# Optimization experiments

Measured on AMD Instinct MI355X. Metric: run time of the kernel, lower is better.

## Reference

```python
import jax, jax.numpy as jnp
import numpy as np

ROPE_THETA = 10000.0

def apply_rope(x, pos):
    # x: [..., h, s, d], pos: [s] int positions
    d = x.shape[-1]
    inv_freq = ROPE_THETA ** (-jnp.arange(0, d, 2, dtype=jnp.float32) / d)  # [d/2]
    ang = pos.astype(jnp.float32)[:, None] * inv_freq[None, :]              # [s, d/2]
    cos, sin = jnp.cos(ang), jnp.sin(ang)
    x1, x2 = x[..., 0::2], x[..., 1::2]
    r1 = x1 * cos - x2 * sin
    r2 = x1 * sin + x2 * cos
    return jnp.stack([r1, r2], axis=-1).reshape(x.shape)

def setup_inputs() -> dict:
    key = jax.random.key(0)
    ks = jax.random.split(key, 5)
    B, S, D = 2, 2048, 1024
    scale = 1.0 / np.sqrt(D)
    return {
        "x": jax.random.normal(ks[0], (B, S, D), dtype=jnp.float32),
        "token_position": jnp.arange(S, dtype=jnp.int32),
        "Wq": jax.random.normal(ks[1], (D, D), dtype=jnp.float32) * scale,
        "Wk": jax.random.normal(ks[2], (D, D), dtype=jnp.float32) * scale,
        "Wv": jax.random.normal(ks[3], (D, D), dtype=jnp.float32) * scale,
        "Wo": jax.random.normal(ks[4], (D, D), dtype=jnp.float32) * scale,
    }

def reference(x, token_position, Wq, Wk, Wv, Wo):
    H = 16
    B, S, D = x.shape
    ds = D // H
    def split_heads(t):  # [b,s,(h d)] -> [b,h,s,d]
        return t.reshape(B, S, H, ds).transpose(0, 2, 1, 3)
    Q = split_heads(x @ Wq.T)
    K = split_heads(x @ Wk.T)
    V = split_heads(x @ Wv.T)
    Q = apply_rope(Q, token_position)
    K = apply_rope(K, token_position)
    scores = jnp.einsum('bhqd,bhkd->bhqk', Q, K) / jnp.sqrt(jnp.float32(ds))
    causal = jnp.tril(jnp.ones((S, S), dtype=bool))
    scores = jnp.where(causal, scores, jnp.finfo(scores.dtype).min)
    attn = jax.nn.softmax(scores, axis=-1)
    out = jnp.einsum('bhqk,bhkd->bhqd', attn, V)
    out = out.transpose(0, 2, 1, 3).reshape(B, S, D)
    return out @ Wo.T
```

## Files before the change

### kernel.cpp

```cpp
#include <hip/hip_runtime.h>
#include <math.h>

#define BB 2
#define SS 2048
#define DD 1024
#define HH 16
#define M_TOTAL (BB*SS)

typedef __attribute__((ext_vector_type(8))) short bf16x8;
typedef __attribute__((ext_vector_type(4))) float f32x4;

__device__ __forceinline__ short f2bf(float f) {
    union { float f; unsigned u; } v; v.f = f;
    unsigned r = v.u + 0x7fffu + ((v.u >> 16) & 1u);
    return (short)(r >> 16);
}
__device__ __forceinline__ float bf2f(short h) {
    union { unsigned u; float f; } v; v.u = ((unsigned)(unsigned short)h) << 16;
    return v.f;
}
__device__ __forceinline__ unsigned cvt_pk_bf16(float lo, float hi) {
    unsigned r;
    asm volatile("v_cvt_pk_bf16_f32 %0, %1, %2" : "=v"(r) : "v"(lo), "v"(hi));
    return r;
}
__device__ __forceinline__ void gload16(const void* g, void* l) {
    __builtin_amdgcn_global_load_lds(
        (const __attribute__((address_space(1))) unsigned int*)g,
        (__attribute__((address_space(3))) unsigned int*)l, 16, 0, 0);
}

__global__ __launch_bounds__(256) void cvt_bf16(const float* __restrict__ in,
                                                short* __restrict__ out, int n,
                                                float scale)
{
    int i = (blockIdx.x * 256 + threadIdx.x) * 4;
    if (i >= n) return;
    float4 v = *(const float4*)(in + i);
    short4 o;
    o.x = f2bf(v.x * scale); o.y = f2bf(v.y * scale);
    o.z = f2bf(v.z * scale); o.w = f2bf(v.w * scale);
    *(short4*)(out + i) = o;
}

template<int BN, int OUT_BF16>
__global__ __launch_bounds__(256) void gemm_nt_mfma(const short* __restrict__ A,
                                                    const short* __restrict__ W0,
                                                    const short* __restrict__ W1,
                                                    const short* __restrict__ W2,
                                                    void* __restrict__ C0,
                                                    void* __restrict__ C1,
                                                    void* __restrict__ C2,
                                                    int M, int N, int K)
{
    constexpr int WC = BN / 64;
    constexpr int WR = 4 / WC;
    constexpr int MW = 128 / WR;
    constexpr int MT = MW / 16;

    __shared__ __align__(16) short As[128 * 64];
    __shared__ __align__(16) short Bs[BN * 64];

    const short* W = (blockIdx.z == 0) ? W0 : (blockIdx.z == 1) ? W1 : W2;
    void* Cout     = (blockIdx.z == 0) ? C0 : (blockIdx.z == 1) ? C1 : C2;

    const int tid = threadIdx.x;
    const int lane = tid & 63;
    const int w = tid >> 6;
    const int lg = lane >> 4, lc = lane & 15;
    const int wr = w / WC, wc = w % WC;
    const int m0 = blockIdx.x * 128, n0 = blockIdx.y * BN;
    const int wbase = (tid & 0xC0) * 8;

    f32x4 acc[MT][4] = {};

    for (int k0 = 0; k0 < K; k0 += 64) {
        __syncthreads();
#pragma unroll
        for (int it = 0; it < 4; ++it) {
            int cl = it * 256 + tid;
            int r = cl >> 3;
            int c = (cl & 7) ^ (r & 7);
            gload16(A + (size_t)(m0 + r) * K + k0 + c * 8, &As[it * 2048 + wbase]);
        }
#pragma unroll
        for (int it = 0; it < BN / 32; ++it) {
            int cl = it * 256 + tid;
            int r = cl >> 3;
            int c = (cl & 7) ^ (r & 7);
            gload16(W + (size_t)(n0 + r) * K + k0 + c * 8, &Bs[it * 2048 + wbase]);
        }
        __syncthreads();
#pragma unroll
        for (int ks = 0; ks < 2; ++ks) {
            bf16x8 af[MT], bfr[4];
#pragma unroll
            for (int mt = 0; mt < MT; ++mt) {
                int row = wr * MW + mt * 16 + lc;
                af[mt] = *(const bf16x8*)&As[row * 64 + (((ks * 4 + lg) ^ (row & 7)) * 8)];
            }
#pragma unroll
            for (int nt = 0; nt < 4; ++nt) {
                int row = wc * 64 + nt * 16 + lc;
                bfr[nt] = *(const bf16x8*)&Bs[row * 64 + (((ks * 4 + lg) ^ (row & 7)) * 8)];
            }
#pragma unroll
            for (int mt = 0; mt < MT; ++mt)
#pragma unroll
                for (int nt = 0; nt < 4; ++nt)
                    acc[mt][nt] = __builtin_amdgcn_mfma_f32_16x16x32_bf16(
                        af[mt], bfr[nt], acc[mt][nt], 0, 0, 0);
        }
    }
#pragma unroll
    for (int mt = 0; mt < MT; ++mt)
#pragma unroll
        for (int nt = 0; nt < 4; ++nt)
#pragma unroll
            for (int rg = 0; rg < 4; ++rg) {
                int row = m0 + wr * MW + mt * 16 + lg * 4 + rg;
                int col = n0 + wc * 64 + nt * 16 + lc;
                if (OUT_BF16)
                    ((short*)Cout)[(size_t)row * N + col] = f2bf(acc[mt][nt][rg]);
                else
                    ((float*)Cout)[(size_t)row * N + col] = acc[mt][nt][rg];
            }
}

__global__ __launch_bounds__(256) void rope_bf16(short* __restrict__ Q,
                                                 short* __restrict__ K,
                                                 const int* __restrict__ pos)
{
    const int t = blockIdx.x * 256 + threadIdx.x;
    const int ig = t & 7;
    const int h = (t >> 3) & 15;
    const int s = (t >> 7) & 2047;
    const int b = t >> 18;
    const float p = (float)pos[s];
    const size_t off = ((size_t)(b * SS + s)) * DD + h * 64 + ig * 8;
    bf16x8 q8 = *(bf16x8*)(Q + off);
    bf16x8 k8 = *(bf16x8*)(K + off);
#pragma unroll
    for (int j = 0; j < 4; ++j) {
        int i = ig * 4 + j;
        float ang = p * __expf(-(float)i * (9.210340371976184f / 32.0f));
        float c = cosf(ang), sn = sinf(ang);
        float q1 = bf2f(q8[2 * j]), q2 = bf2f(q8[2 * j + 1]);
        q8[2 * j]     = f2bf(q1 * c - q2 * sn);
        q8[2 * j + 1] = f2bf(q1 * sn + q2 * c);
        float k1 = bf2f(k8[2 * j]), k2 = bf2f(k8[2 * j + 1]);
        k8[2 * j]     = f2bf(k1 * c - k2 * sn);
        k8[2 * j + 1] = f2bf(k1 * sn + k2 * c);
    }
    *(bf16x8*)(Q + off) = q8;
    *(bf16x8*)(K + off) = k8;
}

__global__ __launch_bounds__(256) void attn_mfma(const short* __restrict__ Q,
                                                 const short* __restrict__ K,
                                                 const short* __restrict__ V,
                                                 short* __restrict__ O)
{
    __shared__ __align__(16) short Ks[2][64 * 64];
    __shared__ __align__(16) unsigned Vt32[2][64 * 36];
    __shared__ __align__(16) unsigned Pl32[4][16 * 36];

    const int tid = threadIdx.x;
    const int lane = tid & 63;
    const int w = tid >> 6;
    const int lg = lane >> 4, lc = lane & 15;

    const int bid = blockIdx.x;
    const int qt = 31 - (bid >> 5);
    const int bh = bid & 31;
    const int b = bh >> 4, h = bh & 15;

    const short* Qh = Q + (size_t)b * SS * DD + h * 64;
    const short* Kh = K + (size_t)b * SS * DD + h * 64;
    const short* Vh = V + (size_t)b * SS * DD + h * 64;
    short* Oh = O + (size_t)b * SS * DD + h * 64;

    const int qg = qt * 64 + w * 16 + lc;
    bf16x8 qa[2];
#pragma unroll
    for (int ks = 0; ks < 2; ++ks)
        qa[ks] = *(const bf16x8*)(Qh + (size_t)qg * DD + ks * 32 + lg * 8);

    f32x4 oaccT[4] = {};
    float l = 0.0f;

    const int vc = tid & 7, vrp = tid >> 3;
    unsigned* Pw = &Pl32[w][0];
    const int kbase_lds = (tid & 0xC0) * 8;

    {
        bf16x8 v0 = *(const bf16x8*)(Vh + (size_t)(2 * vrp) * DD + vc * 8);
        bf16x8 v1 = *(const bf16x8*)(Vh + (size_t)(2 * vrp + 1) * DD + vc * 8);
#pragma unroll
        for (int it = 0; it < 2; ++it) {
            int cl = it * 256 + tid;
            int r = cl >> 3;
            int c = (cl & 7) ^ (r & 7);
            gload16(Kh + (size_t)r * DD + c * 8, &Ks[0][it * 2048 + kbase_lds]);
        }
#pragma unroll
        for (int j = 0; j < 8; ++j) {
            int ds = vc * 8 + j;
            unsigned pk = (unsigned)(unsigned short)v0[j] |
                          ((unsigned)(unsigned short)v1[j] << 16);
            Vt32[0][ds * 36 + (vrp ^ (vc << 2))] = pk;
        }
    }
    __syncthreads();
    int cur = 0;

    for (int kt = 0; kt <= qt; ++kt) {
        bf16x8 v0n, v1n;
        const bool more = (kt < qt);
        if (more) {
            const int nv0 = (kt + 1) * 64;
            v0n = *(const bf16x8*)(Vh + (size_t)(nv0 + 2 * vrp) * DD + vc * 8);
            v1n = *(const bf16x8*)(Vh + (size_t)(nv0 + 2 * vrp + 1) * DD + vc * 8);
#pragma unroll
            for (int it = 0; it < 2; ++it) {
                int cl = it * 256 + tid;
                int r = cl >> 3;
                int c = (cl & 7) ^ (r & 7);
                gload16(Kh + (size_t)(nv0 + r) * DD + c * 8,
                        &Ks[cur ^ 1][it * 2048 + kbase_lds]);
            }
        }

        f32x4 s[4] = {};
        __builtin_amdgcn_s_setprio(1);
#pragma unroll
        for (int ks = 0; ks < 2; ++ks) {
            int c2 = ks * 4 + lg;
#pragma unroll
            for (int t = 0; t < 4; ++t) {
                int kr = t * 16 + lc;
                bf16x8 kb = *(const bf16x8*)&Ks[cur][kr * 64 + ((c2 ^ (kr & 7)) * 8)];
                s[t] = __builtin_amdgcn_mfma_f32_16x16x32_bf16(kb, qa[ks], s[t], 0, 0, 0);
            }
        }
        __builtin_amdgcn_s_setprio(0);

        if (kt == qt) {
            const int kv0 = kt * 64;
#pragma unroll
            for (int t = 0; t < 4; ++t)
#pragma unroll
                for (int rg = 0; rg < 4; ++rg)
                    if (kv0 + t * 16 + lg * 4 + rg > qg) s[t][rg] = -1e30f;
        }

#pragma unroll
        for (int t = 0; t < 4; ++t) {
            float p0 = exp2f(s[t][0] - 16.0f);
            float p1 = exp2f(s[t][1] - 16.0f);
            float p2 = exp2f(s[t][2] - 16.0f);
            float p3 = exp2f(s[t][3] - 16.0f);
            l += (p0 + p1) + (p2 + p3);
            Pw[lc * 36 + 8 * t + 2 * lg]     = cvt_pk_bf16(p0, p1);
            Pw[lc * 36 + 8 * t + 2 * lg + 1] = cvt_pk_bf16(p2, p3);
        }

        __builtin_amdgcn_s_setprio(1);
#pragma unroll
        for (int ks = 0; ks < 2; ++ks) {
            bf16x8 pb = *(const bf16x8*)&Pw[lc * 36 + 16 * ks + 4 * lg];
#pragma unroll
            for (int dt = 0; dt < 4; ++dt) {
                int vr = dt * 16 + lc;
                bf16x8 vb = *(const bf16x8*)&Vt32[cur][vr * 36 +
                                4 * ((ks * 4 + lg) ^ ((vr >> 3) & 7))];
                oaccT[dt] = __builtin_amdgcn_mfma_f32_16x16x32_bf16(vb, pb, oaccT[dt], 0, 0, 0);
            }
        }
        __builtin_amdgcn_s_setprio(0);

        if (more) {
#pragma unroll
            for (int j = 0; j < 8; ++j) {
                int ds = vc * 8 + j;
                unsigned pk = (unsigned)(unsigned short)v0n[j] |
                              ((unsigned)(unsigned short)v1n[j] << 16);
                Vt32[cur ^ 1][ds * 36 + (vrp ^ (vc << 2))] = pk;
            }
        }
        __syncthreads();
        cur ^= 1;
    }

    l += __shfl_xor(l, 16);
    l += __shfl_xor(l, 32);
    const float inv = 1.0f / l;
#pragma unroll
    for (int dt = 0; dt < 4; ++dt)
#pragma unroll
        for (int rg = 0; rg < 4; ++rg)
            Oh[(size_t)qg * DD + dt * 16 + lg * 4 + rg] = f2bf(oaccT[dt][rg] * inv);
}

extern "C" void kernel_launch(void* const* d_in, const int* in_sizes, int n_in,
                              void* d_out, int out_size, void* d_ws, size_t ws_size,
                              hipStream_t stream)
{
    const float* x   = (const float*)d_in[0];
    const int*   pos = (const int*)d_in[1];
    const float* Wq  = (const float*)d_in[2];
    const float* Wk  = (const float*)d_in[3];
    const float* Wv  = (const float*)d_in[4];
    const float* Wo  = (const float*)d_in[5];
    float* out = (float*)d_out;

    const size_t T = (size_t)M_TOTAL * DD;
    const size_t WSZ = (size_t)DD * DD;
    short* xb  = (short*)d_ws;
    short* wqb = xb + T;
    short* wkb = wqb + WSZ;
    short* wvb = wkb + WSZ;
    short* wob = wvb + WSZ;
    short* Qb  = wob + WSZ;
    short* Kb  = Qb + T;
    short* Vb  = Kb + T;
    short* AOb = Vb + T;

    cvt_bf16<<<(int)(T / 1024), 256, 0, stream>>>(x, xb, (int)T, 1.0f);
    cvt_bf16<<<(int)(WSZ / 1024), 256, 0, stream>>>(Wq, wqb, (int)WSZ, 0.18033688011112042f);
    cvt_bf16<<<(int)(WSZ / 1024), 256, 0, stream>>>(Wk, wkb, (int)WSZ, 1.0f);
    cvt_bf16<<<(int)(WSZ / 1024), 256, 0, stream>>>(Wv, wvb, (int)WSZ, 1.0f);
    cvt_bf16<<<(int)(WSZ / 1024), 256, 0, stream>>>(Wo, wob, (int)WSZ, 1.0f);

    dim3 gqkv(M_TOTAL / 128, DD / 128, 3);
    gemm_nt_mfma<128, 1><<<gqkv, 256, 0, stream>>>(
        xb, wqb, wkb, wvb, Qb, Kb, Vb, M_TOTAL, DD, DD);

    rope_bf16<<<(BB * SS * HH * 8) / 256, 256, 0, stream>>>(Qb, Kb, pos);

    attn_mfma<<<BB * HH * (SS / 64), 256, 0, stream>>>(Qb, Kb, Vb, AOb);

    dim3 go(M_TOTAL / 128, DD / 64, 1);
    gemm_nt_mfma<64, 0><<<go, 256, 0, stream>>>(
        AOb, wob, wob, wob, (void*)out, (void*)out, (void*)out, M_TOTAL, DD, DD);
}
```

Measured before the change: 122.0 us.

## Pair causal query tiles per block and fuse bf16 conversion kernels

The attention kernel now has each block process two query tiles, a long one (31-pi) and a short one (pi), so every block does the same amount of causal work. This halves the grid to 512 blocks and aims to remove the tail imbalance. The five fp32-to-bf16 conversion launches are merged into one kernel that picks its source by index range, which saves launch overhead. The constant -16 offset inside exp2f is also removed, which may raise overflow risk if scores are large.

```diff
diff --git a/kernel.cpp b/kernel.cpp
--- a/kernel.cpp
+++ b/kernel.cpp
@@ -30,17 +30,32 @@
         (__attribute__((address_space(3))) unsigned int*)l, 16, 0, 0);
 }
 
-__global__ __launch_bounds__(256) void cvt_bf16(const float* __restrict__ in,
-                                                short* __restrict__ out, int n,
-                                                float scale)
-{
-    int i = (blockIdx.x * 256 + threadIdx.x) * 4;
-    if (i >= n) return;
-    float4 v = *(const float4*)(in + i);
+__global__ __launch_bounds__(256) void cvt_all(const float* __restrict__ x,
+                                               const float* __restrict__ wq,
+                                               const float* __restrict__ wk,
+                                               const float* __restrict__ wv,
+                                               const float* __restrict__ wo,
+                                               short* __restrict__ xb,
+                                               short* __restrict__ wqb,
+                                               short* __restrict__ wkb,
+                                               short* __restrict__ wvb,
+                                               short* __restrict__ wob,
+                                               float qscale)
+{
+    const size_t T = (size_t)M_TOTAL * DD;
+    const size_t W = (size_t)DD * DD;
+    size_t i = ((size_t)blockIdx.x * 256 + threadIdx.x) * 4;
+    const float* src; short* dst; float sc = 1.0f; size_t off;
+    if (i < T)              { src = x;  dst = xb;  off = i; }
+    else if (i < T + W)     { src = wq; dst = wqb; off = i - T; sc = qscale; }
+    else if (i < T + 2*W)   { src = wk; dst = wkb; off = i - T - W; }
+    else if (i < T + 3*W)   { src = wv; dst = wvb; off = i - T - 2*W; }
+    else                    { src = wo; dst = wob; off = i - T - 3*W; }
+    float4 v = *(const float4*)(src + off);
     short4 o;
-    o.x = f2bf(v.x * scale); o.y = f2bf(v.y * scale);
-    o.z = f2bf(v.z * scale); o.w = f2bf(v.w * scale);
-    *(short4*)(out + i) = o;
+    o.x = f2bf(v.x * sc); o.y = f2bf(v.y * sc);
+    o.z = f2bf(v.z * sc); o.w = f2bf(v.w * sc);
+    *(short4*)(dst + off) = o;
 }
 
 template<int BN, int OUT_BF16>
@@ -171,8 +186,8 @@
     const int lg = lane >> 4, lc = lane & 15;
 
     const int bid = blockIdx.x;
-    const int qt = 31 - (bid >> 5);
-    const int bh = bid & 31;
+    const int pi = bid & 15;
+    const int bh = bid >> 4;
     const int b = bh >> 4, h = bh & 15;
 
     const short* Qh = Q + (size_t)b * SS * DD + h * 64;
@@ -180,126 +195,131 @@
     const short* Vh = V + (size_t)b * SS * DD + h * 64;
     short* Oh = O + (size_t)b * SS * DD + h * 64;
 
-    const int qg = qt * 64 + w * 16 + lc;
-    bf16x8 qa[2];
-#pragma unroll
-    for (int ks = 0; ks < 2; ++ks)
-        qa[ks] = *(const bf16x8*)(Qh + (size_t)qg * DD + ks * 32 + lg * 8);
-
-    f32x4 oaccT[4] = {};
-    float l = 0.0f;
-
     const int vc = tid & 7, vrp = tid >> 3;
     unsigned* Pw = &Pl32[w][0];
     const int kbase_lds = (tid & 0xC0) * 8;
 
-    {
-        bf16x8 v0 = *(const bf16x8*)(Vh + (size_t)(2 * vrp) * DD + vc * 8);
-        bf16x8 v1 = *(const bf16x8*)(Vh + (size_t)(2 * vrp + 1) * DD + vc * 8);
-#pragma unroll
-        for (int it = 0; it < 2; ++it) {
-            int cl = it * 256 + tid;
-            int r = cl >> 3;
-            int c = (cl & 7) ^ (r & 7);
-            gload16(Kh + (size_t)r * DD + c * 8, &Ks[0][it * 2048 + kbase_lds]);
-        }
-#pragma unroll
-        for (int j = 0; j < 8; ++j) {
-            int ds = vc * 8 + j;
-            unsigned pk = (unsigned)(unsigned short)v0[j] |
-                          ((unsigned)(unsigned short)v1[j] << 16);
-            Vt32[0][ds * 36 + (vrp ^ (vc << 2))] = pk;
-        }
-    }
-    __syncthreads();
-    int cur = 0;
-
-    for (int kt = 0; kt <= qt; ++kt) {
-        bf16x8 v0n, v1n;
-        const bool more = (kt < qt);
-        if (more) {
-            const int nv0 = (kt + 1) * 64;
-            v0n = *(const bf16x8*)(Vh + (size_t)(nv0 + 2 * vrp) * DD + vc * 8);
-            v1n = *(const bf16x8*)(Vh + (size_t)(nv0 + 2 * vrp + 1) * DD + vc * 8);
+#pragma unroll 1
+    for (int pass = 0; pass < 2; ++pass) {
+        const int qt = pass == 0 ? 31 - pi : pi;
+        const int qg = qt * 64 + w * 16 + lc;
+        bf16x8 qa[2];
+#pragma unroll
+        for (int ks = 0; ks < 2; ++ks)
+            qa[ks] = *(const bf16x8*)(Qh + (size_t)qg * DD + ks * 32 + lg * 8);
+
+        f32x4 oaccT[4] = {};
+        float l = 0.0f;
+
+        {
+            bf16x8 v0 = *(const bf16x8*)(Vh + (size_t)(2 * vrp) * DD + vc * 8);
+            bf16x8 v1 = *(const bf16x8*)(Vh + (size_t)(2 * vrp + 1) * DD + vc * 8);
 #pragma unroll
             for (int it = 0; it < 2; ++it) {
                 int cl = it * 256 + tid;
                 int r = cl >> 3;
                 int c = (cl & 7) ^ (r & 7);
-                gload16(Kh + (size_t)(nv0 + r) * DD + c * 8,
-                        &Ks[cur ^ 1][it * 2048 + kbase_lds]);
-            }
-        }
-
-        f32x4 s[4] = {};
-        __builtin_amdgcn_s_setprio(1);
-#pragma unroll
-        for (int ks = 0; ks < 2; ++ks) {
-            int c2 = ks * 4 + lg;
-#pragma unroll
-            for (int t = 0; t < 4; ++t) {
-                int kr = t * 16 + lc;
-                bf16x8 kb = *(const bf16x8*)&Ks[cur][kr * 64 + ((c2 ^ (kr & 7)) * 8)];
-                s[t] = __builtin_amdgcn_mfma_f32_16x16x32_bf16(kb, qa[ks], s[t], 0, 0, 0);
-            }
-        }
-        __builtin_amdgcn_s_setprio(0);
-
-        if (kt == qt) {
-            const int kv0 = kt * 64;
-#pragma unroll
-            for (int t = 0; t < 4; ++t)
-#pragma unroll
-                for (int rg = 0; rg < 4; ++rg)
-                    if (kv0 + t * 16 + lg * 4 + rg > qg) s[t][rg] = -1e30f;
-        }
-
-#pragma unroll
-        for (int t = 0; t < 4; ++t) {
-            float p0 = exp2f(s[t][0] - 16.0f);
-            float p1 = exp2f(s[t][1] - 16.0f);
-            float p2 = exp2f(s[t][2] - 16.0f);
-            float p3 = exp2f(s[t][3] - 16.0f);
-            l += (p0 + p1) + (p2 + p3);
-            Pw[lc * 36 + 8 * t + 2 * lg]     = cvt_pk_bf16(p0, p1);
-            Pw[lc * 36 + 8 * t + 2 * lg + 1] = cvt_pk_bf16(p2, p3);
-        }
-
-        __builtin_amdgcn_s_setprio(1);
-#pragma unroll
-        for (int ks = 0; ks < 2; ++ks) {
-            bf16x8 pb = *(const bf16x8*)&Pw[lc * 36 + 16 * ks + 4 * lg];
-#pragma unroll
-            for (int dt = 0; dt < 4; ++dt) {
-                int vr = dt * 16 + lc;
-                bf16x8 vb = *(const bf16x8*)&Vt32[cur][vr * 36 +
-                                4 * ((ks * 4 + lg) ^ ((vr >> 3) & 7))];
-                oaccT[dt] = __builtin_amdgcn_mfma_f32_16x16x32_bf16(vb, pb, oaccT[dt], 0, 0, 0);
-            }
-        }
-        __builtin_amdgcn_s_setprio(0);
-
-        if (more) {
+                gload16(Kh + (size_t)r * DD + c * 8, &Ks[0][it * 2048 + kbase_lds]);
+            }
 #pragma unroll
             for (int j = 0; j < 8; ++j) {
                 int ds = vc * 8 + j;
-                unsigned pk = (unsigned)(unsigned short)v0n[j] |
-                              ((unsigned)(unsigned short)v1n[j] << 16);
-                Vt32[cur ^ 1][ds * 36 + (vrp ^ (vc << 2))] = pk;
+                unsigned pk = (unsigned)(unsigned short)v0[j] |
+                              ((unsigned)(unsigned short)v1[j] << 16);
+                Vt32[0][ds * 36 + (vrp ^ (vc << 2))] = pk;
             }
         }
         __syncthreads();
-        cur ^= 1;
+        int cur = 0;
+
+        for (int kt = 0; kt <= qt; ++kt) {
+            bf16x8 v0n, v1n;
+            const bool more = (kt < qt);
+            if (more) {
+                const int nv0 = (kt + 1) * 64;
+                v0n = *(const bf16x8*)(Vh + (size_t)(nv0 + 2 * vrp) * DD + vc * 8);
+                v1n = *(const bf16x8*)(Vh + (size_t)(nv0 + 2 * vrp + 1) * DD + vc * 8);
+#pragma unroll
+                for (int it = 0; it < 2; ++it) {
+                    int cl = it * 256 + tid;
+                    int r = cl >> 3;
+                    int c = (cl & 7) ^ (r & 7);
+                    gload16(Kh + (size_t)(nv0 + r) * DD + c * 8,
+                            &Ks[cur ^ 1][it * 2048 + kbase_lds]);
+                }
+            }
+
+            f32x4 s[4] = {};
+            __builtin_amdgcn_s_setprio(1);
+#pragma unroll
+            for (int ks = 0; ks < 2; ++ks) {
+                int c2 = ks * 4 + lg;
+#pragma unroll
+                for (int t = 0; t < 4; ++t) {
+                    int kr = t * 16 + lc;
+                    bf16x8 kb = *(const bf16x8*)&Ks[cur][kr * 64 + ((c2 ^ (kr & 7)) * 8)];
+                    s[t] = __builtin_amdgcn_mfma_f32_16x16x32_bf16(kb, qa[ks], s[t], 0, 0, 0);
+                }
+            }
+            __builtin_amdgcn_s_setprio(0);
+
+            if (kt == qt) {
+                const int kv0 = kt * 64;
+#pragma unroll
+                for (int t = 0; t < 4; ++t)
+#pragma unroll
+                    for (int rg = 0; rg < 4; ++rg)
+                        if (kv0 + t * 16 + lg * 4 + rg > qg) s[t][rg] = -1e30f;
+            }
+
+#pragma unroll
+            for (int t = 0; t < 4; ++t) {
+                float p0 = exp2f(s[t][0]);
+                float p1 = exp2f(s[t][1]);
+                float p2 = exp2f(s[t][2]);
+                float p3 = exp2f(s[t][3]);
+                l += (p0 + p1) + (p2 + p3);
+                Pw[lc * 36 + 8 * t + 2 * lg]     = cvt_pk_bf16(p0, p1);
+                Pw[lc * 36 + 8 * t + 2 * lg + 1] = cvt_pk_bf16(p2, p3);
+            }
+
+            __builtin_amdgcn_s_setprio(1);
+#pragma unroll
+            for (int ks = 0; ks < 2; ++ks) {
+                bf16x8 pb = *(const bf16x8*)&Pw[lc * 36 + 16 * ks + 4 * lg];
+#pragma unroll
+                for (int dt = 0; dt < 4; ++dt) {
+                    int vr = dt * 16 + lc;
+                    bf16x8 vb = *(const bf16x8*)&Vt32[cur][vr * 36 +
+                                    4 * ((ks * 4 + lg) ^ ((vr >> 3) & 7))];
+                    oaccT[dt] = __builtin_amdgcn_mfma_f32_16x16x32_bf16(vb, pb, oaccT[dt], 0, 0, 0);
+                }
+            }
+            __builtin_amdgcn_s_setprio(0);
+
+            if (more) {
+#pragma unroll
+                for (int j = 0; j < 8; ++j) {
+                    int ds = vc * 8 + j;
+                    unsigned pk = (unsigned)(unsigned short)v0n[j] |
+                                  ((unsigned)(unsigned short)v1n[j] << 16);
+                    Vt32[cur ^ 1][ds * 36 + (vrp ^ (vc << 2))] = pk;
+                }
+            }
+            __syncthreads();
+            cur ^= 1;
+        }
+
+        l += __shfl_xor(l, 16);
+        l += __shfl_xor(l, 32);
+        const float inv = 1.0f / l;
+#pragma unroll
+        for (int dt = 0; dt < 4; ++dt)
+#pragma unroll
+            for (int rg = 0; rg < 4; ++rg)
+                Oh[(size_t)qg * DD + dt * 16 + lg * 4 + rg] = f2bf(oaccT[dt][rg] * inv);
+        __syncthreads();
     }
-
-    l += __shfl_xor(l, 16);
-    l += __shfl_xor(l, 32);
-    const float inv = 1.0f / l;
-#pragma unroll
-    for (int dt = 0; dt < 4; ++dt)
-#pragma unroll
-        for (int rg = 0; rg < 4; ++rg)
-            Oh[(size_t)qg * DD + dt * 16 + lg * 4 + rg] = f2bf(oaccT[dt][rg] * inv);
 }
 
 extern "C" void kernel_launch(void* const* d_in, const int* in_sizes, int n_in,
@@ -326,11 +346,10 @@
     short* Vb  = Kb + T;
     short* AOb = Vb + T;
 
-    cvt_bf16<<<(int)(T / 1024), 256, 0, stream>>>(x, xb, (int)T, 1.0f);
-    cvt_bf16<<<(int)(WSZ / 1024), 256, 0, stream>>>(Wq, wqb, (int)WSZ, 0.18033688011112042f);
-    cvt_bf16<<<(int)(WSZ / 1024), 256, 0, stream>>>(Wk, wkb, (int)WSZ, 1.0f);
-    cvt_bf16<<<(int)(WSZ / 1024), 256, 0, stream>>>(Wv, wvb, (int)WSZ, 1.0f);
-    cvt_bf16<<<(int)(WSZ / 1024), 256, 0, stream>>>(Wo, wob, (int)WSZ, 1.0f);
+    const int cvt_blocks = (int)((T + 4 * WSZ) / 1024);
+    cvt_all<<<cvt_blocks, 256, 0, stream>>>(x, Wq, Wk, Wv, Wo,
+                                            xb, wqb, wkb, wvb, wob,
+                                            0.18033688011112042f);
 
     dim3 gqkv(M_TOTAL / 128, DD / 128, 3);
     gemm_nt_mfma<128, 1><<<gqkv, 256, 0, stream>>>(
@@ -338,7 +357,7 @@
 
     rope_bf16<<<(BB * SS * HH * 8) / 256, 256, 0, stream>>>(Qb, Kb, pos);
 
-    attn_mfma<<<BB * HH * (SS / 64), 256, 0, stream>>>(Qb, Kb, Vb, AOb);
+    attn_mfma<<<BB * HH * (SS / 128), 256, 0, stream>>>(Qb, Kb, Vb, AOb);
 
     dim3 go(M_TOTAL / 128, DD / 64, 1);
     gemm_nt_mfma<64, 0><<<go, 256, 0, stream>>>(
```

After: 121.2 us. Within noise of the previous version (-0.6%).
